# Kernel tuning notes

Measured on AMD Instinct MI355X. Metric: run time of the kernel, lower is better.

The kernel has to match this reference:

```python
import jax, jax.numpy as jnp
import numpy as np
from jax.scipy.special import gammaln

# sizes (see shape_source)
N_CELLS = 1024
N_GENES = 1000
N_LATENT = 50
NB_ENC = 16          # encoder histogram bins per gene
NB_DEC = 16          # decoder mixture components (sum(n_decoder_bins))
N_HID = 16           # encoder hidden dim
N_CUTS = 4_000_000
N_FRAGS = 2_000_000
N_TOTAL_CELLS = 10_000
N_TOTAL_CUTS = 50_000_000
BN_EPS = 1e-5


def _normal_logprob(x, loc, scale):
    z = (x - loc) / scale
    return -0.5 * z * z - jnp.log(scale) - 0.5 * jnp.log(2.0 * jnp.pi)


def setup_inputs() -> dict:
    key = jax.random.key(0)
    ks = jax.random.split(key, 20)
    cut_coordinates = jax.random.uniform(ks[0], (N_CUTS,), dtype=jnp.float32)
    cut_cell = jax.random.randint(ks[1], (N_CUTS,), 0, N_CELLS)
    cut_local_gene_ix = jax.random.randint(ks[2], (N_CUTS,), 0, N_GENES)
    cut_local_cellxgene_ix = cut_cell * N_GENES + cut_local_gene_ix
    local_cellxgene_ix = jax.random.randint(ks[3], (N_FRAGS,), 0, N_CELLS * N_GENES)
    genes_oi = jnp.arange(N_GENES)
    cells_oi = jnp.arange(N_CELLS)
    eps = jax.random.normal(ks[4], (N_CELLS, N_LATENT), dtype=jnp.float32)
    n_in = N_GENES * NB_ENC
    enc_W1 = jax.random.normal(ks[5], (n_in, N_HID)) * (1.0 / np.sqrt(n_in))
    enc_b1 = jnp.zeros((N_HID,))
    bn_gamma = jnp.ones((N_HID,))
    bn_beta = jnp.zeros((N_HID,))
    W_loc = jax.random.normal(ks[6], (N_HID, N_LATENT)) * (1.0 / np.sqrt(N_HID))
    b_loc = jnp.zeros((N_LATENT,))
    W_scale = jax.random.normal(ks[7], (N_HID, N_LATENT)) * (1.0 / np.sqrt(N_HID))
    b_scale = jnp.zeros((N_LATENT,))
    logit_weight = jax.random.normal(ks[8], (N_GENES, N_LATENT, NB_DEC)) * 0.05
    rho_weight = jax.random.normal(ks[9], (N_GENES, N_LATENT)) * 0.05
    baseline_heights = jax.random.normal(ks[10], (N_GENES, NB_DEC)) * 0.1
    libsize = jax.random.randint(ks[11], (N_TOTAL_CELLS,), 1000, 20000)
    rho_bias = jax.random.uniform(ks[12], (N_GENES,), minval=1e-4, maxval=1e-2)
    return dict(
        cut_coordinates=cut_coordinates, eps=eps,
        enc_W1=enc_W1, enc_b1=enc_b1, bn_gamma=bn_gamma, bn_beta=bn_beta,
        W_loc=W_loc, b_loc=b_loc, W_scale=W_scale, b_scale=b_scale,
        logit_weight=logit_weight, rho_weight=rho_weight,
        baseline_heights=baseline_heights, rho_bias=rho_bias,
        cut_local_cellxgene_ix=cut_local_cellxgene_ix,
        cut_local_gene_ix=cut_local_gene_ix,
        local_cellxgene_ix=local_cellxgene_ix,
        genes_oi=genes_oi, cells_oi=cells_oi, libsize=libsize,
    )


def reference(cut_coordinates, eps, enc_W1, enc_b1, bn_gamma, bn_beta,
              W_loc, b_loc, W_scale, b_scale, logit_weight, rho_weight,
              baseline_heights, rho_bias, cut_local_cellxgene_ix,
              cut_local_gene_ix, local_cellxgene_ix, genes_oi, cells_oi,
              libsize):
    n_cells = cells_oi.shape[0]
    n_genes = genes_oi.shape[0]

    # ---- Encoder: digitize + bincount histogram ----
    bin_enc = jnp.minimum(jnp.floor(cut_coordinates * NB_ENC), NB_ENC - 1).astype(jnp.int32)
    digitized = bin_enc + cut_local_cellxgene_ix.astype(jnp.int32) * NB_ENC
    counts = jax.ops.segment_sum(jnp.ones_like(cut_coordinates), digitized,
                                 num_segments=n_cells * n_genes * NB_ENC)
    x = jnp.log1p(counts.reshape(n_cells, n_genes * NB_ENC))  # [C, G*NB]

    h = x @ enc_W1 + enc_b1
    mu = h.mean(axis=0)
    var = h.var(axis=0)  # biased, matches torch BN in train mode
    h = (h - mu) / jnp.sqrt(var + BN_EPS) * bn_gamma + bn_beta
    h = jax.nn.relu(h)
    loc = h @ W_loc + b_loc                 # [C, L]
    scale = jnp.exp(h @ W_scale + b_scale)  # [C, L]

    # ---- latent sample + KL ----
    q_scale = scale * 0.1
    latent = loc + q_scale * eps
    latent_kl = (_normal_logprob(latent, 0.0, 1.0)
                 - _normal_logprob(latent, loc, q_scale)) * (N_TOTAL_CELLS / n_cells)

    # ---- Decoder (n_layers=0: per-gene linear heads) ----
    lw = logit_weight[genes_oi]                       # [G, L, K]
    rw = rho_weight[genes_oi]                         # [G, L]
    mixture_delta = jnp.einsum('cl,glk->cgk', latent, lw)  # [C, G, K]
    rho_delta = jnp.einsum('cl,gl->cg', latent, rw)        # [C, G]
    md_cxg = mixture_delta.reshape(n_cells * n_genes, NB_DEC)
    md_cut = md_cxg[cut_local_cellxgene_ix]           # [N_CUTS, K] gather
    mixture_delta_kl = _normal_logprob(lw, 0.0, 0.1)

    # ---- mixture likelihood: piecewise-constant spline density per cut ----
    logits = baseline_heights[cut_local_gene_ix] + md_cut  # [N_CUTS, K]
    logp = jax.nn.log_softmax(logits, axis=-1)
    bin_dec = jnp.minimum(jnp.floor(cut_coordinates * NB_DEC), NB_DEC - 1).astype(jnp.int32)
    likelihood_mixture = (jnp.take_along_axis(logp, bin_dec[:, None], axis=1)[:, 0]
                          + jnp.log(float(NB_DEC)))

    # ---- fragment-count Poisson likelihood ----
    fragexpr = (rho_bias[genes_oi][None, :] * jnp.exp(rho_delta)
                * libsize[cells_oi].astype(jnp.float32)[:, None])  # [C, G]
    fragmentcounts = jax.ops.segment_sum(
        jnp.ones((local_cellxgene_ix.shape[0],), jnp.float32),
        local_cellxgene_ix, num_segments=n_cells * n_genes
    ).reshape(n_cells, n_genes)
    likelihood_frag = (fragmentcounts * jnp.log(fragexpr) - fragexpr
                       - gammaln(fragmentcounts + 1.0))

    rho_delta_kl = _normal_logprob(rw, 0.0, 0.1)

    likelihood = (likelihood_mixture.sum() * (N_TOTAL_CUTS / cut_coordinates.shape[0])
                  + likelihood_frag.sum() * (N_TOTAL_CELLS / n_cells))
    elbo = (-likelihood - latent_kl.sum() - mixture_delta_kl.sum()
            - rho_delta_kl.sum())
    return elbo
```

## Files before the change

kernel.cpp:

```cpp
#include <hip/hip_runtime.h>
#include <hip/hip_bf16.h>
#include <math.h>


#define G_      1000
#define C_      1024
#define L_      50
#define K_      16
#define NHID_   16
#define CUT_SCALE   12.5f
#define CELL_SCALE  9.765625f

#define CHUNK_    6144
#define RCAP_CUT  18432
#define RCAP_FRAG 9216

#define GCNTC_OFF  0ull
#define GCNTF_OFF  1024ull
#define DONE_OFF   2048ull
#define DACC_OFF   6400ull
#define HT_OFF     6912ull
#define ZERO_BYTES 72448ull
#define LATBF_OFF  72448ull
#define LWT_OFF    203520ull
#define ENTC_OFF   2251520ull
#define ENTF_OFF   11688704ull
#define MERGED_OFF 16407296ull
#define FRAGU8_OFF 24599296ull
#define LATT_OFF   25623296ull
#define WS_NEED    25828096ull

typedef __attribute__((ext_vector_type(8))) short short8;
typedef __attribute__((ext_vector_type(4))) float f32x4;

__device__ __constant__ float LGT[32] = {
    0.0f, 0.0f, 0.6931471805599453f, 1.791759469228055f, 3.1780538303479458f,
    4.787491742782046f, 6.579251212010101f, 8.525161361065415f,
    10.60460290274525f, 12.801827480081469f, 15.104412573075516f,
    17.502307845873887f, 19.987214495661885f, 22.552163853123425f,
    25.19122118273868f, 27.89927138384089f, 30.671860106080672f,
    33.50507345013689f, 36.39544520803305f, 39.339884187199495f,
    42.335616460753485f, 45.38013889847691f, 48.47118135183523f,
    51.60667556776438f, 54.78472939811232f, 58.00360522298052f,
    61.261701761002f, 64.55753862700633f, 67.88974313718154f,
    71.25703896716801f, 74.65823634883016f, 78.0922235533153f };

__device__ __forceinline__ double atomAddF64(double* p, double v) {
    return __hip_atomic_fetch_add(p, v, __ATOMIC_RELAXED,
                                  __HIP_MEMORY_SCOPE_AGENT);
}

__device__ __forceinline__ float block_sum_256(float v) {
    __shared__ float sm[256];
    int t = threadIdx.x;
    __syncthreads();
    sm[t] = v;
    __syncthreads();
#pragma unroll
    for (int s = 128; s > 0; s >>= 1) {
        if (t < s) sm[t] += sm[t + s];
        __syncthreads();
    }
    return sm[0];
}

__global__ __launch_bounds__(256)
void part_kernel(const int* __restrict__ cut_ix,
                 const float* __restrict__ coord,
                 const int* __restrict__ frag_ix,
                 unsigned int* __restrict__ gcnt_c,
                 unsigned int* __restrict__ gcnt_f,
                 unsigned short* __restrict__ entc,
                 unsigned short* __restrict__ entf,
                 const float* __restrict__ lw,
                 const float* __restrict__ rw,
                 __hip_bfloat16* __restrict__ lwT,
                 double* __restrict__ dacc,
                 int n_cuts, int n_frags, int ncc, int nblk_part) {
    int t = threadIdx.x;
    int bid = blockIdx.x;
    if (bid >= nblk_part) {
        int r = bid - nblk_part;
        if (r < 256) {
            for (int g = r; g < G_; g += 256) {
                for (int i = t; i < L_ * K_; i += 256) {
                    float v = lw[(size_t)g * (L_ * K_) + i];
                    lwT[(size_t)g * 1024 + (i & 15) * 64 + (i >> 4)] =
                        __float2bfloat16(v);
                }
                for (int i = t; i < 16 * 14; i += 256) {
                    int n = i / 14, l = 50 + (i % 14);
                    lwT[(size_t)g * 1024 + n * 64 + l] = __float2bfloat16(0.f);
                }
            }
        } else {
            const int NTOT = G_ * L_ * K_ + G_ * L_;
            int wb = r - 256;
            float s = 0.f;
            for (int i = wb * 256 + t; i < NTOT; i += 256 * 256) {
                float w = (i < G_ * L_ * K_) ? lw[i] : rw[i - G_ * L_ * K_];
                s += fmaf(-50.f * w, w, 1.3836465597893733f);
            }
            s = block_sum_256(s);
            if (t == 0) atomAddF64(&dacc[wb & 63], (double)(-s));
        }
        return;
    }
    __shared__ unsigned int cnt[256], excl[256], cur[256], gbas[256];
    __shared__ unsigned short stage[CHUNK_];
    __shared__ unsigned char bkof[CHUNK_];
    bool isCut = (bid < ncc);
    int blk = isCut ? bid : bid - ncc;
    const int* idx = isCut ? cut_ix : frag_ix;
    int n = isCut ? n_cuts : n_frags;
    int rcap = isCut ? RCAP_CUT : RCAP_FRAG;
    unsigned int* gcount = isCut ? gcnt_c : gcnt_f;
    unsigned short* ent = isCut ? entc : entf;
    int i0 = blk * CHUNK_;
    cnt[t] = 0;
    int4 I[6]; float4 X[6];
    unsigned int vm;
    bool full = (i0 + CHUNK_ <= n);
    if (full) {
        const int4* ip = (const int4*)(idx + i0);
#pragma unroll
        for (int k = 0; k < 6; ++k) I[k] = ip[k * 256 + t];
        if (isCut) {
            const float4* xp = (const float4*)(coord + i0);
#pragma unroll
            for (int k = 0; k < 6; ++k) X[k] = xp[k * 256 + t];
        }
        vm = 0xFFFFFFu;
    } else {
        vm = 0;
#pragma unroll
        for (int k = 0; k < 6; ++k) {
            int r0 = i0 + (k * 256 + t) * 4;
            int* Ii = (int*)&I[k]; float* Xi = (float*)&X[k];
#pragma unroll
            for (int u = 0; u < 4; ++u) {
                bool v = (r0 + u) < n;
                if (v) vm |= 1u << (k * 4 + u);
                Ii[u] = v ? idx[r0 + u] : 0;
                Xi[u] = (v && isCut) ? coord[r0 + u] : 0.f;
            }
        }
    }
    __syncthreads();
#pragma unroll
    for (int k = 0; k < 6; ++k) {
        const int* Ii = (const int*)&I[k];
        const float* Xi = (const float*)&X[k];
#pragma unroll
        for (int u = 0; u < 4; ++u) {
            if (vm & (1u << (k * 4 + u))) {
                int ix = Ii[u];
                int c = ix / G_;
                int g = ix - c * G_;
                unsigned int bk;
                if (isCut) {
                    int b = (int)(Xi[u] * 16.f); b = b > 15 ? 15 : b;
                    bk = ((unsigned)(c >> 6) << 4) | ((unsigned)(g * K_ + b) >> 10);
                } else {
                    bk = ((unsigned)(c >> 6) << 4) | ((unsigned)g >> 6);
                }
                atomicAdd(&cnt[bk], 1u);
            }
        }
    }
    __syncthreads();
    if (t < 64) {
        unsigned int c0 = cnt[t * 4 + 0], c1 = cnt[t * 4 + 1];
        unsigned int c2 = cnt[t * 4 + 2], c3 = cnt[t * 4 + 3];
        unsigned int tot = c0 + c1 + c2 + c3;
        unsigned int run = tot;
#pragma unroll
        for (int o = 1; o < 64; o <<= 1) {
            unsigned int v = __shfl_up(run, o, 64);
            if (t >= o) run += v;
        }
        unsigned int base = run - tot;
        excl[t * 4 + 0] = base;
        excl[t * 4 + 1] = base + c0;
        excl[t * 4 + 2] = base + c0 + c1;
        excl[t * 4 + 3] = base + c0 + c1 + c2;
    }
    __syncthreads();
    gbas[t] = cnt[t] ? atomicAdd(&gcount[t], cnt[t]) : 0u;
    cur[t] = excl[t];
    __syncthreads();
#pragma unroll
    for (int k = 0; k < 6; ++k) {
        const int* Ii = (const int*)&I[k];
        const float* Xi = (const float*)&X[k];
#pragma unroll
        for (int u = 0; u < 4; ++u) {
            if (vm & (1u << (k * 4 + u))) {
                int ix = Ii[u];
                int c = ix / G_;
                int g = ix - c * G_;
                unsigned int bk; unsigned short e;
                if (isCut) {
                    int b = (int)(Xi[u] * 16.f); b = b > 15 ? 15 : b;
                    int bin = g * K_ + b;
                    bk = ((unsigned)(c >> 6) << 4) | ((unsigned)bin >> 10);
                    e = (unsigned short)(((c & 63) << 10) | (bin & 1023));
                } else {
                    bk = ((unsigned)(c >> 6) << 4) | ((unsigned)g >> 6);
                    e = (unsigned short)(((c & 63) << 6) | (g & 63));
                }
                unsigned int p = atomicAdd(&cur[bk], 1u);
                stage[p] = e;
                bkof[p] = (unsigned char)bk;
            }
        }
    }
    __syncthreads();
    int total = n - i0; if (total > CHUNK_) total = CHUNK_;
    for (int p = t; p < total; p += 256) {
        unsigned int bk = bkof[p];
        unsigned int dst = gbas[bk] + (p - excl[bk]);
        if (dst < (unsigned)rcap)
            ent[(size_t)bk * rcap + dst] = stage[p];
    }
}

__global__ __launch_bounds__(256)
void mid_kernel(const unsigned int* __restrict__ gcnt_c,
                const unsigned short* __restrict__ entc,
                const unsigned int* __restrict__ gcnt_f,
                const unsigned short* __restrict__ entf,
                const float* __restrict__ W1,
                unsigned int* __restrict__ merged,
                unsigned int* __restrict__ fragw,
                float* __restrict__ hT) {
    __shared__ unsigned int h[4096];
    int t = threadIdx.x;
    int bid = blockIdx.x;
    if (bid < 1024) {
        int bk = bid >> 2, q = bid & 3;
        int cg = bk >> 4, bc = bk & 15;
        for (int i = t; i < 2048; i += 256) h[i] = 0;
        __syncthreads();
        unsigned int count = gcnt_c[bk];
        if (count > RCAP_CUT) count = RCAP_CUT;
        const unsigned int* e32 = (const unsigned int*)(entc + (size_t)bk * RCAP_CUT);
        unsigned int npair = count >> 1;
        for (unsigned int base = 0; base < npair; base += 1024) {
            unsigned int w[4]; bool val[4];
#pragma unroll
            for (int u = 0; u < 4; ++u) {
                unsigned int p = base + u * 256 + t;
                val[u] = (p < npair);
                w[u] = val[u] ? e32[p] : 0u;
            }
#pragma unroll
            for (int u = 0; u < 4; ++u) {
                if (val[u]) {
                    unsigned int v0 = w[u] & 0xffffu, v1 = w[u] >> 16;
                    unsigned int b0 = v0 & 1023u, b1 = v1 & 1023u;
                    if ((int)(b0 >> 8) == q) {
                        unsigned int c0 = v0 >> 10;
                        atomicAdd(&h[(b0 & 255u) * 8 + (c0 >> 3)],
                                  1u << ((c0 & 7) * 4));
                    }
                    if ((int)(b1 >> 8) == q) {
                        unsigned int c1 = v1 >> 10;
                        atomicAdd(&h[(b1 & 255u) * 8 + (c1 >> 3)],
                                  1u << ((c1 & 7) * 4));
                    }
                }
            }
        }
        if (t == 0 && (count & 1u)) {
            unsigned int v = ((const unsigned short*)e32)[count - 1];
            unsigned int b0 = v & 1023u;
            if ((int)(b0 >> 8) == q) {
                unsigned int c0 = v >> 10;
                atomicAdd(&h[(b0 & 255u) * 8 + (c0 >> 3)], 1u << ((c0 & 7) * 4));
            }
        }
        __syncthreads();
        for (int i = t; i < 2048; i += 256) {
            int bin = bc * 1024 + q * 256 + (i >> 3);
            if (bin < 16000)
                merged[(unsigned)bin * 128u + (unsigned)cg * 8u + (i & 7)] = h[i];
        }
        int c_lo = t & 63, sub = t >> 6;
        float acc[NHID_];
#pragma unroll
        for (int j = 0; j < NHID_; ++j) acc[j] = 0.f;
        int rbase = bc * 1024 + q * 256 + sub * 64;
        int sh = (c_lo & 7) * 4;
#pragma unroll 2
        for (int bl = 0; bl < 64; ++bl) {
            int row = rbase + bl;
            if (row < 16000) {
                int rl = sub * 64 + bl;
                unsigned int w = h[rl * 8 + (c_lo >> 3)];
                float xv = __logf((float)(((w >> sh) & 0xfu) + 1u));
                const float4* wr = (const float4*)
                    (W1 + (size_t)__builtin_amdgcn_readfirstlane(row) * NHID_);
                float4 wa = wr[0];
                float4 wb = wr[1];
                float4 wc = wr[2];
                float4 wd = wr[3];
                acc[0] = fmaf(xv, wa.x, acc[0]);  acc[1] = fmaf(xv, wa.y, acc[1]);
                acc[2] = fmaf(xv, wa.z, acc[2]);  acc[3] = fmaf(xv, wa.w, acc[3]);
                acc[4] = fmaf(xv, wb.x, acc[4]);  acc[5] = fmaf(xv, wb.y, acc[5]);
                acc[6] = fmaf(xv, wb.z, acc[6]);  acc[7] = fmaf(xv, wb.w, acc[7]);
                acc[8] = fmaf(xv, wc.x, acc[8]);  acc[9] = fmaf(xv, wc.y, acc[9]);
                acc[10] = fmaf(xv, wc.z, acc[10]); acc[11] = fmaf(xv, wc.w, acc[11]);
                acc[12] = fmaf(xv, wd.x, acc[12]); acc[13] = fmaf(xv, wd.y, acc[13]);
                acc[14] = fmaf(xv, wd.z, acc[14]); acc[15] = fmaf(xv, wd.w, acc[15]);
            }
        }
        __syncthreads();
        float* sp = (float*)h;
#pragma unroll
        for (int j = 0; j < NHID_; ++j) sp[sub * 1024 + j * 64 + c_lo] = acc[j];
        __syncthreads();
        for (int i = t; i < 1024; i += 256) {
            int j = i >> 6, c = i & 63;
            float v = sp[j * 64 + c] + sp[1024 + j * 64 + c]
                    + sp[2048 + j * 64 + c] + sp[3072 + j * 64 + c];
            atomicAdd(&hT[j * C_ + cg * 64 + c], v);
        }
    } else {
        int bk = bid - 1024, cg = bk >> 4, gc = bk & 15;
        for (int i = t; i < 2048; i += 256) h[i] = 0;
        __syncthreads();
        unsigned int count = gcnt_f[bk];
        if (count > RCAP_FRAG) count = RCAP_FRAG;
        const unsigned short* e = entf + (size_t)bk * RCAP_FRAG;
#pragma unroll 4
        for (unsigned int p = t; p < count; p += 256) {
            unsigned int v = e[p];
            unsigned int g_lo = v & 63u;
            unsigned int c_lo = v >> 6;
            atomicAdd(&h[g_lo * 32 + (c_lo >> 1)], 1u << ((c_lo & 1) * 16));
        }
        __syncthreads();
        for (int i = t; i < 1024; i += 256) {
            int g_lo = i >> 4, wb = i & 15;
            unsigned int lo = h[g_lo * 32 + wb * 2];
            unsigned int hi = h[g_lo * 32 + wb * 2 + 1];
            unsigned int outv = (lo & 0xffu) | (((lo >> 16) & 0xffu) << 8)
                              | ((hi & 0xffu) << 16) | (((hi >> 16) & 0xffu) << 24);
            int g = gc * 64 + g_lo;
            if (g < G_)
                fragw[(unsigned)g * 256u + (unsigned)cg * 16u + wb] = outv;
        }
    }
}

__global__ __launch_bounds__(256)
void latent_kernel(const float* __restrict__ hT,
                   const float* __restrict__ gamma,
                   const float* __restrict__ beta,
                   const float* __restrict__ W_loc,
                   const float* __restrict__ b_loc,
                   const float* __restrict__ W_scale,
                   const float* __restrict__ b_scale,
                   const float* __restrict__ eps,
                   float* __restrict__ latT,
                   __hip_bfloat16* __restrict__ latbf,
                   double* __restrict__ dacc) {
    __shared__ float scs[NHID_], shs[NHID_];
    int t = threadIdx.x;
    {
        int j = t >> 4, cl = t & 15;
        double s1 = 0.0, s2 = 0.0;
#pragma unroll 8
        for (int k = 0; k < 64; ++k) {
            float v = hT[j * C_ + cl + k * 16];
            s1 += (double)v; s2 += (double)v * (double)v;
        }
#pragma unroll
        for (int m = 1; m < 16; m <<= 1) {
            s1 += __shfl_xor(s1, m);
            s2 += __shfl_xor(s2, m);
        }
        if (cl == 0) {
            double mean = s1 * (1.0 / C_);
            double var = s2 * (1.0 / C_) - mean * mean;
            float rstd = rsqrtf((float)var + 1e-5f);
            float sc = gamma[j] * rstd;
            scs[j] = sc;
            shs[j] = beta[j] - (float)mean * sc;
        }
    }
    __syncthreads();
    int idx = blockIdx.x * 256 + t;
    float kl = 0.f;
    {
        int c = idx / L_;
        int l = idx - c * L_;
        float hb[NHID_];
#pragma unroll
        for (int j = 0; j < NHID_; ++j) {
            float v = fmaf(hT[j * C_ + c], scs[j], shs[j]);
            hb[j] = v > 0.f ? v : 0.f;
        }
        float loc = b_loc[l], ls = b_scale[l];
#pragma unroll
        for (int j = 0; j < NHID_; ++j) {
            loc = fmaf(hb[j], W_loc[j * L_ + l], loc);
            ls  = fmaf(hb[j], W_scale[j * L_ + l], ls);
        }
        float qs = 0.1f * __expf(ls);
        float e = eps[idx];
        float lat = fmaf(qs, e, loc);
        latT[(size_t)l * C_ + c] = lat;
        latbf[c * 64 + l] = __float2bfloat16(lat);
        if (l < 14) latbf[c * 64 + 50 + l] = __float2bfloat16(0.f);
        float z = (lat - loc) / qs;
        kl = fmaf(-0.5f * lat, lat, fmaf(0.5f * z, z, __logf(qs)));
    }
    float s = block_sum_256(kl);
    if (threadIdx.x == 0)
        atomAddF64(&dacc[blockIdx.x & 63], (double)(-CELL_SCALE * s));
}

__global__ __launch_bounds__(256)
void mixpois_kernel(const __hip_bfloat16* __restrict__ latbf,
                    const __hip_bfloat16* __restrict__ lwT,
                    const unsigned int* __restrict__ merged,
                    const float* __restrict__ baseline,
                    const float* __restrict__ latT,
                    const float* __restrict__ rw,
                    const float* __restrict__ rho_bias,
                    const int* __restrict__ libsize,
                    const unsigned char* __restrict__ fragb,
                    double* __restrict__ dacc,
                    unsigned int* __restrict__ done,
                    float* __restrict__ out) {
    int g = blockIdx.x;
    float contrib;
    if (blockIdx.y < 4) {
        int lane = threadIdx.x & 63;
        int wv = threadIdx.x >> 6;
        int n = lane & 15;
        int quad = lane >> 4;
        const __hip_bfloat16* bb = lwT + (size_t)g * 1024 + n * 64 + quad * 8;
        short8 b1 = *(const short8*)bb;
        short8 b2 = *(const short8*)(bb + 32);
        float bl = baseline[g * K_ + n];
        float partial = 0.f;
        int cwave = blockIdx.y * 256 + wv * 64;
#pragma unroll
        for (int mt = 0; mt < 4; ++mt) {
            int c0 = cwave + mt * 16;
            const __hip_bfloat16* aa = latbf + (size_t)(c0 + n) * 64 + quad * 8;
            short8 a1 = *(const short8*)aa;
            short8 a2 = *(const short8*)(aa + 32);
            f32x4 d = {bl, bl, bl, bl};
            d = __builtin_amdgcn_mfma_f32_16x16x32_bf16(a1, b1, d, 0, 0, 0);
            d = __builtin_amdgcn_mfma_f32_16x16x32_bf16(a2, b2, d, 0, 0, 0);
            float mx[4], ex[4];
#pragma unroll
            for (int r = 0; r < 4; ++r) mx[r] = d[r];
#pragma unroll
            for (int m = 1; m < 16; m <<= 1)
#pragma unroll
                for (int r = 0; r < 4; ++r)
                    mx[r] = fmaxf(mx[r], __shfl_xor(mx[r], m));
#pragma unroll
            for (int r = 0; r < 4; ++r) ex[r] = __expf(d[r] - mx[r]);
#pragma unroll
            for (int m = 1; m < 16; m <<= 1)
#pragma unroll
                for (int r = 0; r < 4; ++r) ex[r] += __shfl_xor(ex[r], m);
            int cp = c0 + quad * 4;
            unsigned int hw =
                merged[(unsigned)(g * K_ + n) * 128u + ((unsigned)cp >> 3)];
            int sb = (cp & 7) * 4;
#pragma unroll
            for (int r = 0; r < 4; ++r) {
                float lse = mx[r] + __logf(ex[r]);
                float cnt = (float)((hw >> (sb + r * 4)) & 0xfu);
                partial = fmaf(cnt, d[r] - lse, partial);
            }
        }
        contrib = block_sum_256(-CUT_SCALE * partial);
    } else {
        int yc = blockIdx.y - 4;
        int c = yc * 256 + threadIdx.x;
        const float* rwg = rw + (size_t)g * L_;
        float rho = 0.f;
#pragma unroll 10
        for (int l = 0; l < L_; ++l)
            rho = fmaf(latT[l * C_ + c], rwg[l], rho);
        unsigned int fc = fragb[(size_t)g * C_ + c];
        float fe = rho_bias[g] * __expf(rho) * (float)libsize[c];
        float lf = fmaf((float)fc, __logf(fe), -fe) - LGT[fc > 31u ? 31u : fc];
        contrib = block_sum_256(-CELL_SCALE * lf);
    }
    __shared__ int lastflag;
    if (threadIdx.x == 0) {
        lastflag = 0;
        int slot = blockIdx.x & 63;
        double oldv = atomAddF64(&dacc[slot], (double)contrib);
        unsigned inc = 1u;
        float dep = (float)oldv;
        asm volatile("" : "+v"(inc) : "v"(dep));
        unsigned quota = ((slot < 40) ? 16u : 15u) * 8u;
        if (atomicAdd(&done[slot * 16], inc) == quota - 1u) {
            if (atomicAdd(&done[1024], 1u) == 63u) lastflag = 1;
        }
    }
    __syncthreads();
    if (lastflag) {
        int t = threadIdx.x;
        if (t < 64) {
            double v = atomAddF64(&dacc[t], 0.0);
#pragma unroll
            for (int m = 1; m < 64; m <<= 1) v += __shfl_xor(v, m);
            if (t == 0)
                out[0] = (float)(v - 138629436.11198905);
        }
    }
}

extern "C" void kernel_launch(void* const* d_in, const int* in_sizes, int n_in,
                              void* d_out, int out_size, void* d_ws, size_t ws_size,
                              hipStream_t stream) {
    const float* cut_coord = (const float*)d_in[0];
    const float* eps       = (const float*)d_in[1];
    const float* enc_W1    = (const float*)d_in[2];
    const float* bn_gamma  = (const float*)d_in[4];
    const float* bn_beta   = (const float*)d_in[5];
    const float* W_loc     = (const float*)d_in[6];
    const float* b_loc     = (const float*)d_in[7];
    const float* W_scale   = (const float*)d_in[8];
    const float* b_scale   = (const float*)d_in[9];
    const float* logit_w   = (const float*)d_in[10];
    const float* rho_w     = (const float*)d_in[11];
    const float* baseline  = (const float*)d_in[12];
    const float* rho_bias  = (const float*)d_in[13];
    const int* cut_cxg     = (const int*)d_in[14];
    const int* frag_ix     = (const int*)d_in[16];
    const int* libsize     = (const int*)d_in[19];

    int n_cuts  = in_sizes[0];
    int n_frags = in_sizes[16];

    char* ws = (char*)d_ws;
    unsigned int*   gcnt_c = (unsigned int*)(ws + GCNTC_OFF);
    unsigned int*   gcnt_f = (unsigned int*)(ws + GCNTF_OFF);
    unsigned int*   done   = (unsigned int*)(ws + DONE_OFF);
    double*         dacc   = (double*)(ws + DACC_OFF);
    float*          hT     = (float*)(ws + HT_OFF);
    __hip_bfloat16* latbf  = (__hip_bfloat16*)(ws + LATBF_OFF);
    __hip_bfloat16* lwT    = (__hip_bfloat16*)(ws + LWT_OFF);
    unsigned short* entc   = (unsigned short*)(ws + ENTC_OFF);
    unsigned short* entf   = (unsigned short*)(ws + ENTF_OFF);
    unsigned int*   merged = (unsigned int*)(ws + MERGED_OFF);
    unsigned int*   fragw  = (unsigned int*)(ws + FRAGU8_OFF);
    float*          latT   = (float*)(ws + LATT_OFF);
    float*          out    = (float*)d_out;

    int ncc = (n_cuts + CHUNK_ - 1) / CHUNK_;
    int ncf = (n_frags + CHUNK_ - 1) / CHUNK_;
    int nblk_part = ncc + ncf;

    hipMemsetAsync(ws, 0, ZERO_BYTES, stream);

    part_kernel<<<nblk_part + 512, 256, 0, stream>>>(
        cut_cxg, cut_coord, frag_ix, gcnt_c, gcnt_f, entc, entf,
        logit_w, rho_w, lwT, dacc,
        n_cuts, n_frags, ncc, nblk_part);
    mid_kernel<<<1280, 256, 0, stream>>>(
        gcnt_c, entc, gcnt_f, entf, enc_W1, merged, fragw, hT);
    latent_kernel<<<(C_ * L_) / 256, 256, 0, stream>>>(
        hT, bn_gamma, bn_beta, W_loc, b_loc, W_scale, b_scale,
        eps, latT, latbf, dacc);
    mixpois_kernel<<<dim3(G_, 8), 256, 0, stream>>>(
        latbf, lwT, merged, baseline, latT, rho_w, rho_bias, libsize,
        (const unsigned char*)fragw, dacc, done, out);
}
```

Baseline: 244.4 us.

## Fuse mixture and Poisson blocks, transpose MFMA operands, stage W1 in LDS

The mixture-likelihood and Poisson-likelihood halves of mixpois_kernel, which previously ran as separate grid rows, now run in the same block, halving the grid and the number of block reductions and atomics. The MFMA operands are swapped so each lane holds four mixture components of one cell. The softmax reductions then need only two cross-lane shuffles instead of four per value. In mid_kernel, the block's slice of W1 is staged into shared memory up front instead of being read row by row from global memory, at the cost of 16 KB more LDS per block, which may lower occupancy.

```diff
diff --git a/kernel.cpp b/kernel.cpp
--- a/kernel.cpp
+++ b/kernel.cpp
@@ -235,11 +235,19 @@
                 unsigned int* __restrict__ fragw,
                 float* __restrict__ hT) {
     __shared__ unsigned int h[4096];
+    __shared__ float w1s[4096];
     int t = threadIdx.x;
     int bid = blockIdx.x;
     if (bid < 1024) {
         int bk = bid >> 2, q = bid & 3;
         int cg = bk >> 4, bc = bk & 15;
+        int wbase = (bc * 1024 + q * 256) * NHID_;
+#pragma unroll
+        for (int r = 0; r < 16; ++r) {
+            int i = r * 256 + t;
+            int gi = wbase + i;
+            w1s[i] = (gi < 16000 * NHID_) ? W1[gi] : 0.f;
+        }
         for (int i = t; i < 2048; i += 256) h[i] = 0;
         __syncthreads();
         unsigned int count = gcnt_c[bk];
@@ -292,6 +300,7 @@
         for (int j = 0; j < NHID_; ++j) acc[j] = 0.f;
         int rbase = bc * 1024 + q * 256 + sub * 64;
         int sh = (c_lo & 7) * 4;
+        const float4* w1v = (const float4*)w1s;
 #pragma unroll 2
         for (int bl = 0; bl < 64; ++bl) {
             int row = rbase + bl;
@@ -299,12 +308,10 @@
                 int rl = sub * 64 + bl;
                 unsigned int w = h[rl * 8 + (c_lo >> 3)];
                 float xv = __logf((float)(((w >> sh) & 0xfu) + 1u));
-                const float4* wr = (const float4*)
-                    (W1 + (size_t)__builtin_amdgcn_readfirstlane(row) * NHID_);
-                float4 wa = wr[0];
-                float4 wb = wr[1];
-                float4 wc = wr[2];
-                float4 wd = wr[3];
+                float4 wa = w1v[rl * 4 + 0];
+                float4 wb = w1v[rl * 4 + 1];
+                float4 wc = w1v[rl * 4 + 2];
+                float4 wd = w1v[rl * 4 + 3];
                 acc[0] = fmaf(xv, wa.x, acc[0]);  acc[1] = fmaf(xv, wa.y, acc[1]);
                 acc[2] = fmaf(xv, wa.z, acc[2]);  acc[3] = fmaf(xv, wa.w, acc[3]);
                 acc[4] = fmaf(xv, wb.x, acc[4]);  acc[5] = fmaf(xv, wb.y, acc[5]);
@@ -436,56 +443,50 @@
                     unsigned int* __restrict__ done,
                     float* __restrict__ out) {
     int g = blockIdx.x;
-    float contrib;
-    if (blockIdx.y < 4) {
-        int lane = threadIdx.x & 63;
-        int wv = threadIdx.x >> 6;
-        int n = lane & 15;
-        int quad = lane >> 4;
-        const __hip_bfloat16* bb = lwT + (size_t)g * 1024 + n * 64 + quad * 8;
-        short8 b1 = *(const short8*)bb;
-        short8 b2 = *(const short8*)(bb + 32);
-        float bl = baseline[g * K_ + n];
-        float partial = 0.f;
-        int cwave = blockIdx.y * 256 + wv * 64;
-#pragma unroll
-        for (int mt = 0; mt < 4; ++mt) {
-            int c0 = cwave + mt * 16;
-            const __hip_bfloat16* aa = latbf + (size_t)(c0 + n) * 64 + quad * 8;
-            short8 a1 = *(const short8*)aa;
-            short8 a2 = *(const short8*)(aa + 32);
-            f32x4 d = {bl, bl, bl, bl};
-            d = __builtin_amdgcn_mfma_f32_16x16x32_bf16(a1, b1, d, 0, 0, 0);
-            d = __builtin_amdgcn_mfma_f32_16x16x32_bf16(a2, b2, d, 0, 0, 0);
-            float mx[4], ex[4];
-#pragma unroll
-            for (int r = 0; r < 4; ++r) mx[r] = d[r];
-#pragma unroll
-            for (int m = 1; m < 16; m <<= 1)
-#pragma unroll
-                for (int r = 0; r < 4; ++r)
-                    mx[r] = fmaxf(mx[r], __shfl_xor(mx[r], m));
-#pragma unroll
-            for (int r = 0; r < 4; ++r) ex[r] = __expf(d[r] - mx[r]);
-#pragma unroll
-            for (int m = 1; m < 16; m <<= 1)
-#pragma unroll
-                for (int r = 0; r < 4; ++r) ex[r] += __shfl_xor(ex[r], m);
-            int cp = c0 + quad * 4;
-            unsigned int hw =
-                merged[(unsigned)(g * K_ + n) * 128u + ((unsigned)cp >> 3)];
-            int sb = (cp & 7) * 4;
-#pragma unroll
-            for (int r = 0; r < 4; ++r) {
-                float lse = mx[r] + __logf(ex[r]);
-                float cnt = (float)((hw >> (sb + r * 4)) & 0xfu);
-                partial = fmaf(cnt, d[r] - lse, partial);
-            }
-        }
-        contrib = block_sum_256(-CUT_SCALE * partial);
-    } else {
-        int yc = blockIdx.y - 4;
-        int c = yc * 256 + threadIdx.x;
+    int y = blockIdx.y;
+    int t = threadIdx.x;
+    int lane = t & 63;
+    int wv = t >> 6;
+    int s16 = lane & 15;
+    int quad = lane >> 4;
+    const __hip_bfloat16* bb = lwT + (size_t)g * 1024 + s16 * 64 + quad * 8;
+    short8 lw1 = *(const short8*)bb;
+    short8 lw2 = *(const short8*)(bb + 32);
+    const float4 bl4 = *(const float4*)(baseline + g * K_ + quad * 4);
+    const unsigned int* mrow =
+        merged + (size_t)(g * K_ + quad * 4) * 128u;
+    float partial = 0.f;
+    int cwave = y * 256 + wv * 64;
+#pragma unroll
+    for (int mt = 0; mt < 4; ++mt) {
+        int c0 = cwave + mt * 16;
+        const __hip_bfloat16* aa = latbf + (size_t)(c0 + s16) * 64 + quad * 8;
+        short8 la1 = *(const short8*)aa;
+        short8 la2 = *(const short8*)(aa + 32);
+        f32x4 d = {bl4.x, bl4.y, bl4.z, bl4.w};
+        d = __builtin_amdgcn_mfma_f32_16x16x32_bf16(lw1, la1, d, 0, 0, 0);
+        d = __builtin_amdgcn_mfma_f32_16x16x32_bf16(lw2, la2, d, 0, 0, 0);
+        float m = fmaxf(fmaxf(d[0], d[1]), fmaxf(d[2], d[3]));
+        m = fmaxf(m, __shfl_xor(m, 16));
+        m = fmaxf(m, __shfl_xor(m, 32));
+        float e0 = __expf(d[0] - m), e1 = __expf(d[1] - m);
+        float e2 = __expf(d[2] - m), e3 = __expf(d[3] - m);
+        float S = (e0 + e1) + (e2 + e3);
+        S += __shfl_xor(S, 16);
+        S += __shfl_xor(S, 32);
+        float lse = m + __logf(S);
+        int cp = c0 + s16;
+        unsigned int widx = (unsigned)cp >> 3;
+        int sb = (cp & 7) * 4;
+#pragma unroll
+        for (int r = 0; r < 4; ++r) {
+            float cnt = (float)((mrow[r * 128u + widx] >> sb) & 0xfu);
+            partial = fmaf(cnt, d[r] - lse, partial);
+        }
+    }
+    float v;
+    {
+        int c = y * 256 + t;
         const float* rwg = rw + (size_t)g * L_;
         float rho = 0.f;
 #pragma unroll 10
@@ -494,8 +495,9 @@
         unsigned int fc = fragb[(size_t)g * C_ + c];
         float fe = rho_bias[g] * __expf(rho) * (float)libsize[c];
         float lf = fmaf((float)fc, __logf(fe), -fe) - LGT[fc > 31u ? 31u : fc];
-        contrib = block_sum_256(-CELL_SCALE * lf);
-    }
+        v = fmaf(-CUT_SCALE, partial, -CELL_SCALE * lf);
+    }
+    float contrib = block_sum_256(v);
     __shared__ int lastflag;
     if (threadIdx.x == 0) {
         lastflag = 0;
@@ -504,20 +506,19 @@
         unsigned inc = 1u;
         float dep = (float)oldv;
         asm volatile("" : "+v"(inc) : "v"(dep));
-        unsigned quota = ((slot < 40) ? 16u : 15u) * 8u;
+        unsigned quota = ((slot < 40) ? 16u : 15u) * 4u;
         if (atomicAdd(&done[slot * 16], inc) == quota - 1u) {
             if (atomicAdd(&done[1024], 1u) == 63u) lastflag = 1;
         }
     }
     __syncthreads();
     if (lastflag) {
-        int t = threadIdx.x;
         if (t < 64) {
-            double v = atomAddF64(&dacc[t], 0.0);
-#pragma unroll
-            for (int m = 1; m < 64; m <<= 1) v += __shfl_xor(v, m);
+            double dv = atomAddF64(&dacc[t], 0.0);
+#pragma unroll
+            for (int m = 1; m < 64; m <<= 1) dv += __shfl_xor(dv, m);
             if (t == 0)
-                out[0] = (float)(v - 138629436.11198905);
+                out[0] = (float)(dv - 138629436.11198905);
         }
     }
 }
@@ -575,7 +576,7 @@
     latent_kernel<<<(C_ * L_) / 256, 256, 0, stream>>>(
         hT, bn_gamma, bn_beta, W_loc, b_loc, W_scale, b_scale,
         eps, latT, latbf, dacc);
-    mixpois_kernel<<<dim3(G_, 8), 256, 0, stream>>>(
+    mixpois_kernel<<<dim3(G_, 4), 256, 0, stream>>>(
         latbf, lwT, merged, baseline, latT, rho_w, rho_bias, libsize,
         (const unsigned char*)fragw, dacc, done, out);
 }
```

Result: faster. 230.5 us (-5.7%).
